# Kernel optimization log

Hardware: AMD Instinct MI355X
Metric: run time of the kernel (lower is better)

The kernel has to match this reference:

```python
import jax, jax.numpy as jnp
import numpy as np

N_HEAD = 16
ROPE_BASE = 10000.0


def rope_cos_sin(T, head_dim, dtype):
    inv_freq = 1.0 / (ROPE_BASE ** (jnp.arange(0, head_dim, 2, dtype=jnp.float32) / head_dim))
    t = jnp.arange(T, dtype=jnp.float32)
    freqs = jnp.einsum('i,j->ij', t, inv_freq)          # [T, head_dim/2]
    emb = jnp.concatenate([freqs, freqs], axis=-1)       # [T, head_dim]
    return jnp.cos(emb).astype(dtype), jnp.sin(emb).astype(dtype)


def rotate_half(x):
    h = x.shape[-1] // 2
    return jnp.concatenate([-x[..., h:], x[..., :h]], axis=-1)


def setup_inputs() -> dict:
    key = jax.random.key(0)
    ks = jax.random.split(key, 5)
    B, T, C = 2, 1024, 2048
    s = 0.02
    return {
        'x': jax.random.normal(ks[0], (B, T, C), dtype=jnp.float32),
        'Wq': jax.random.normal(ks[1], (C, C), dtype=jnp.float32) * s,
        'Wk': jax.random.normal(ks[2], (C, C), dtype=jnp.float32) * s,
        'Wv': jax.random.normal(ks[3], (C, C), dtype=jnp.float32) * s,
        'Wo': jax.random.normal(ks[4], (C, C), dtype=jnp.float32) * s,
    }


def reference(x, Wq, Wk, Wv, Wo):
    B, T, C = x.shape
    H = N_HEAD
    D = C // H
    # torch Linear: y = x @ W.T  (W is [out, in])
    q = jnp.einsum('btc,oc->bto', x, Wq).reshape(B, T, H, D).transpose(0, 2, 1, 3)
    k = jnp.einsum('btc,oc->bto', x, Wk).reshape(B, T, H, D).transpose(0, 2, 1, 3)
    v = jnp.einsum('btc,oc->bto', x, Wv).reshape(B, T, H, D).transpose(0, 2, 1, 3)
    cos, sin = rope_cos_sin(T, D, x.dtype)               # [T, D]
    cos = cos[None, None]                                 # [1,1,T,D]
    sin = sin[None, None]
    q = q * cos + rotate_half(q) * sin
    k = k * cos + rotate_half(k) * sin
    scale = 1.0 / jnp.sqrt(jnp.asarray(D, dtype=x.dtype))
    att = jnp.einsum('bhqd,bhkd->bhqk', q, k) * scale    # [B,H,T,T]
    causal = jnp.tril(jnp.ones((T, T), dtype=bool))
    att = jnp.where(causal[None, None], att, jnp.finfo(x.dtype).min)
    att = jax.nn.softmax(att, axis=-1)
    y = jnp.einsum('bhqk,bhkd->bhqd', att, v)            # [B,H,T,D]
    y = y.transpose(0, 2, 1, 3).reshape(B, T, C)
    return jnp.einsum('btc,oc->bto', y, Wo)
```

## Files before the change

### kernel.cpp

```cpp
#include <hip/hip_runtime.h>
#include <stdint.h>

typedef unsigned short u16;
typedef __bf16 bf16x8 __attribute__((ext_vector_type(8)));
typedef float  f32x4  __attribute__((ext_vector_type(4)));

#define B_  2
#define T_  1024
#define C_  2048
#define H_  16
#define D_  128
#define NTENS 4194304

__device__ __forceinline__ u16 f2bf(float f) {
    union { float f; uint32_t u; } v; v.f = f;
    uint32_t r = (v.u + 0x7FFFu + ((v.u >> 16) & 1u)) >> 16;
    return (u16)r;
}
__device__ __forceinline__ float bf2f(u16 h) {
    union { uint32_t u; float f; } v; v.u = ((uint32_t)h) << 16;
    return v.f;
}

__global__ __launch_bounds__(256) void k_convert(
    const float* __restrict__ x, const float* __restrict__ wq,
    const float* __restrict__ wk, const float* __restrict__ wv,
    const float* __restrict__ wo, u16* __restrict__ dst,
    float* __restrict__ ct, float* __restrict__ st)
{
    int z = blockIdx.z;
    if (z == 5) {
        int idx = blockIdx.x * 256 + threadIdx.x;
        if (idx < 65536) {
            int t = idx >> 6, d = idx & 63;
            float inv = expf(-(float)d * (9.210340371976184f / 64.0f));
            float th = (float)t * inv;
            float s, c;
            sincosf(th, &s, &c);
            ct[idx] = c;
            st[idx] = s;
        }
        return;
    }
    const float* src = (z == 0) ? x : (z == 1) ? wq : (z == 2) ? wk : (z == 3) ? wv : wo;
    u16* d = dst + (size_t)z * NTENS;
    size_t i = ((size_t)blockIdx.x * 256 + threadIdx.x) * 4;
    float4 v = *(const float4*)(src + i);
    ushort4 o;
    o.x = f2bf(v.x); o.y = f2bf(v.y); o.z = f2bf(v.z); o.w = f2bf(v.w);
    *(ushort4*)(d + i) = o;
}

__global__ __launch_bounds__(256) void k_transpose_v(
    const u16* __restrict__ vb, u16* __restrict__ vt)
{
    __shared__ u16 L[64 * 136];
    int t0 = blockIdx.x << 6;
    int bh = blockIdx.y, b = bh >> 4, h = bh & 15;
    const u16* src = vb + (size_t)b * (T_ * C_) + h * D_;
    u16* dst = vt + (size_t)bh * (D_ * T_);
    int tid = threadIdx.x;
#pragma unroll
    for (int i = 0; i < 4; ++i) {
        int idx = (i << 8) + tid;
        int r = idx >> 4, s = idx & 15;
        *(uint4*)&L[r * 136 + (s << 3)] =
            *(const uint4*)&src[(size_t)(t0 + r) * C_ + (s << 3)];
    }
    __syncthreads();
#pragma unroll
    for (int i = 0; i < 8; ++i) {
        int idx = (i << 8) + tid;
        int d = idx >> 4, s = idx & 15;
        int t = s << 2;
        ushort4 o;
        o.x = L[(t    ) * 136 + d];
        o.y = L[(t + 1) * 136 + d];
        o.z = L[(t + 2) * 136 + d];
        o.w = L[(t + 3) * 136 + d];
        *(ushort4*)&dst[(size_t)d * T_ + t0 + t] = o;
    }
}

template<int MTILE, int EPI>
__device__ __forceinline__ void gemm_tile_nt(
    const u16* __restrict__ A, int lda,
    const u16* __restrict__ Bp, int ldb,
    void* __restrict__ Cp, int ldc,
    int m0, int n0, int K,
    u16* SMEM, const float* __restrict__ ct, const float* __restrict__ st, int z)
{
    constexpr int MF  = MTILE / 16;
    constexpr int ACH = MTILE / 32;
    u16* As = SMEM;
    u16* Bs = SMEM + MTILE * 64;

    const int tid  = threadIdx.x;
    const int wave = tid >> 6;
    const int lane = tid & 63;
    const int frow = lane & 15;
    const int quad = lane >> 4;

    const int lrow8  = lane >> 3;
    const int slot   = lane & 7;
    const int gchunk = slot ^ lrow8;

    f32x4 acc[MF][2] = {};

    size_t aoff[ACH], boff[4];
#pragma unroll
    for (int i = 0; i < ACH; ++i) {
        int c = (i << 2) + wave;
        int r = (c << 3) + lrow8;
        aoff[i] = (size_t)(m0 + r) * lda + (gchunk << 3);
    }
#pragma unroll
    for (int i = 0; i < 4; ++i) {
        int r = (i << 5) + (wave << 3) + lrow8;
        boff[i] = (size_t)(n0 + r) * ldb + (gchunk << 3);
    }

    for (int kt = 0; kt < K; kt += 64) {
#pragma unroll
        for (int i = 0; i < ACH; ++i) {
            int c = (i << 2) + wave;
            __builtin_amdgcn_global_load_lds(
                (const __attribute__((address_space(1))) void*)(A + aoff[i] + kt),
                (__attribute__((address_space(3))) void*)(As + (c << 9)), 16, 0, 0);
        }
#pragma unroll
        for (int i = 0; i < 4; ++i) {
            int c = (i << 2) + wave;
            __builtin_amdgcn_global_load_lds(
                (const __attribute__((address_space(1))) void*)(Bp + boff[i] + kt),
                (__attribute__((address_space(3))) void*)(Bs + (c << 9)), 16, 0, 0);
        }
        __syncthreads();

#pragma unroll
        for (int ks = 0; ks < 2; ++ks) {
            int lk = (ks << 2) + quad;
            bf16x8 af[MF], bfv[2];
#pragma unroll
            for (int i = 0; i < MF; ++i) {
                int ar = (i << 4) + frow;
                af[i] = *(const bf16x8*)&As[ar * 64 + ((lk ^ (frow & 7)) << 3)];
            }
#pragma unroll
            for (int j = 0; j < 2; ++j) {
                int br = (wave << 4) + (j << 6) + frow;
                bfv[j] = *(const bf16x8*)&Bs[br * 64 + ((lk ^ (frow & 7)) << 3)];
            }
#pragma unroll
            for (int i = 0; i < MF; ++i)
#pragma unroll
                for (int j = 0; j < 2; ++j)
                    acc[i][j] = __builtin_amdgcn_mfma_f32_16x16x32_bf16(
                        af[i], bfv[j], acc[i][j], 0, 0, 0);
        }
        __syncthreads();
    }

    if constexpr (EPI == 2) {
        if (z < 2) {
            const int d = (wave << 4) + frow;
            const float sc = (z == 0) ? 0.08838834764831845f : 1.0f;
            u16* Op = (u16*)Cp;
#pragma unroll
            for (int i = 0; i < MF; ++i)
#pragma unroll
                for (int r = 0; r < 4; ++r) {
                    int m = m0 + (i << 4) + (quad << 2) + r;
                    int t = m & 1023;
                    float c = ct[t * 64 + d], s = st[t * 64 + d];
                    float a = acc[i][0][r], bb = acc[i][1][r];
                    Op[(size_t)m * ldc + n0 + d]      = f2bf((a * c - bb * s) * sc);
                    Op[(size_t)m * ldc + n0 + d + 64] = f2bf((bb * c + a * s) * sc);
                }
            return;
        }
    }

#pragma unroll
    for (int i = 0; i < MF; ++i)
#pragma unroll
        for (int j = 0; j < 2; ++j)
#pragma unroll
            for (int r = 0; r < 4; ++r) {
                int m = m0 + (i << 4) + (quad << 2) + r;
                int n = n0 + (wave << 4) + (j << 6) + frow;
                if constexpr (EPI == 0)
                    ((float*)Cp)[(size_t)m * ldc + n] = acc[i][j][r];
                else
                    ((u16*)Cp)[(size_t)m * ldc + n] = f2bf(acc[i][j][r]);
            }
}

__global__ __launch_bounds__(256) void k_gemm_qkv(
    const u16* __restrict__ xb, const u16* __restrict__ wq,
    const u16* __restrict__ wk, const u16* __restrict__ wv,
    u16* __restrict__ q, u16* __restrict__ k, u16* __restrict__ v,
    const float* __restrict__ ct, const float* __restrict__ st)
{
    __shared__ u16 SMEM[64 * 64 + 128 * 64];
    int z = blockIdx.z;
    const u16* Bp = (z == 0) ? wq : (z == 1) ? wk : wv;
    u16* Op       = (z == 0) ? q  : (z == 1) ? k  : v;
    gemm_tile_nt<64, 2>(xb, C_, Bp, C_, Op, C_,
                        blockIdx.y * 64, blockIdx.x * 128, C_, SMEM, ct, st, z);
}

__global__ __launch_bounds__(256) void k_flash(
    const u16* __restrict__ qb, const u16* __restrict__ kb,
    const u16* __restrict__ vt, u16* __restrict__ yb)
{
    __shared__ u16 Ks[128 * 128];
    __shared__ u16 Vs[128 * 128];

    const int bx  = blockIdx.x;
    const int bh  = bx & 31, b = bh >> 4, h = bh & 15;
    const int qt  = (bx < 256) ? (15 - (bx >> 5)) : ((bx >> 5) - 8);
    const int KT  = (qt >> 1) + 1;
    const int tid = threadIdx.x, wave = tid >> 6, lane = tid & 63;
    const int frow = lane & 15, quad = lane >> 4;

    const u16* qbase = qb + (size_t)b * (T_ * C_) + h * D_;
    const u16* kbase = kb + (size_t)b * (T_ * C_) + h * D_;
    const u16* vbase = vt + (size_t)bh * (D_ * T_);
    const int q0 = qt << 6;

    bf16x8 qf[4];
#pragma unroll
    for (int ks = 0; ks < 4; ++ks)
        qf[ks] = *(const bf16x8*)&qbase[(size_t)(q0 + (wave << 4) + frow) * C_
                                        + (ks << 5) + (quad << 3)];

    f32x4 Y[8] = {};
    float mrow[4], lrow[4];
#pragma unroll
    for (int r = 0; r < 4; ++r) { mrow[r] = -3e38f; lrow[r] = 0.f; }

    const int tok = q0 + (wave << 4) + (quad << 2);

    for (int kt = 0; kt < KT; ++kt) {
        const int k0 = kt << 7;
        {
            const int r4 = lane >> 4, s16 = lane & 15;
#pragma unroll
            for (int i = 0; i < 8; ++i) {
                int c = (i << 2) + wave;
                int row = (c << 2) + r4;
                int g = (s16 & 8) | ((s16 & 7) ^ (row & 7));
                __builtin_amdgcn_global_load_lds(
                    (const __attribute__((address_space(1))) void*)(kbase + (size_t)(k0 + row) * C_ + (g << 3)),
                    (__attribute__((address_space(3))) void*)(Ks + (c << 9)), 16, 0, 0);
                __builtin_amdgcn_global_load_lds(
                    (const __attribute__((address_space(1))) void*)(vbase + (size_t)row * T_ + k0 + (g << 3)),
                    (__attribute__((address_space(3))) void*)(Vs + (c << 9)), 16, 0, 0);
            }
        }
        __syncthreads();

        f32x4 S[8] = {};
#pragma unroll
        for (int ks = 0; ks < 4; ++ks) {
            int lk = (ks << 2) + quad;
            int sw = ((lk & 8) | ((lk & 7) ^ (frow & 7))) << 3;
#pragma unroll
            for (int jj = 0; jj < 8; ++jj) {
                bf16x8 bb = *(const bf16x8*)&Ks[((jj << 4) + frow) * 128 + sw];
                S[jj] = __builtin_amdgcn_mfma_f32_16x16x32_bf16(qf[ks], bb, S[jj], 0, 0, 0);
            }
        }

        if (kt == KT - 1) {
#pragma unroll
            for (int jj = 0; jj < 8; ++jj) {
                int colg = k0 + (jj << 4) + frow;
#pragma unroll
                for (int r = 0; r < 4; ++r)
                    if (colg > tok + r) S[jj][r] = -1e30f;
            }
        }

        float al[4];
#pragma unroll
        for (int r = 0; r < 4; ++r) {
            float tm = -3e38f;
#pragma unroll
            for (int jj = 0; jj < 8; ++jj) tm = fmaxf(tm, S[jj][r]);
#pragma unroll
            for (int off = 8; off > 0; off >>= 1) tm = fmaxf(tm, __shfl_xor(tm, off));
            float mn = fmaxf(mrow[r], tm);
            al[r] = __expf(mrow[r] - mn);
            mrow[r] = mn;
            float rs = 0.f;
#pragma unroll
            for (int jj = 0; jj < 8; ++jj) {
                float e = __expf(S[jj][r] - mn);
                S[jj][r] = e;
                rs += e;
            }
#pragma unroll
            for (int off = 8; off > 0; off >>= 1) rs += __shfl_xor(rs, off);
            lrow[r] = lrow[r] * al[r] + rs;
        }
#pragma unroll
        for (int dj = 0; dj < 8; ++dj)
#pragma unroll
            for (int r = 0; r < 4; ++r) Y[dj][r] *= al[r];

        __syncthreads();

        u16* Ps = Ks;
#pragma unroll
        for (int jj = 0; jj < 8; ++jj)
#pragma unroll
            for (int r = 0; r < 4; ++r)
                Ps[((wave << 4) + (quad << 2) + r) * 136 + (jj << 4) + frow] = f2bf(S[jj][r]);

#pragma unroll
        for (int ks = 0; ks < 4; ++ks) {
            bf16x8 pa = *(const bf16x8*)&Ps[((wave << 4) + frow) * 136 + (ks << 5) + (quad << 3)];
            int lk = (ks << 2) + quad;
            int sw = ((lk & 8) | ((lk & 7) ^ (frow & 7))) << 3;
#pragma unroll
            for (int dj = 0; dj < 8; ++dj) {
                bf16x8 vv = *(const bf16x8*)&Vs[((dj << 4) + frow) * 128 + sw];
                Y[dj] = __builtin_amdgcn_mfma_f32_16x16x32_bf16(pa, vv, Y[dj], 0, 0, 0);
            }
        }
        __syncthreads();
    }

    u16* ybase = yb + (size_t)b * (T_ * C_) + h * D_;
#pragma unroll
    for (int r = 0; r < 4; ++r) {
        float inv = 1.0f / lrow[r];
#pragma unroll
        for (int dj = 0; dj < 8; ++dj)
            ybase[(size_t)(tok + r) * C_ + (dj << 4) + frow] = f2bf(Y[dj][r] * inv);
    }
}

__global__ __launch_bounds__(256) void k_gemm_out(
    const u16* __restrict__ yb, const u16* __restrict__ wo, float* __restrict__ out)
{
    __shared__ u16 SMEM[64 * 64 + 128 * 64];
    gemm_tile_nt<64, 0>(yb, C_, wo, C_, out, C_,
                        blockIdx.y * 64, blockIdx.x * 128, C_, SMEM, nullptr, nullptr, 0);
}

extern "C" void kernel_launch(void* const* d_in, const int* in_sizes, int n_in,
                              void* d_out, int out_size, void* d_ws, size_t ws_size,
                              hipStream_t stream)
{
    (void)in_sizes; (void)n_in; (void)out_size; (void)ws_size;
    const float* x  = (const float*)d_in[0];
    const float* Wq = (const float*)d_in[1];
    const float* Wk = (const float*)d_in[2];
    const float* Wv = (const float*)d_in[3];
    const float* Wo = (const float*)d_in[4];

    u16* ws  = (u16*)d_ws;
    u16* xb  = ws;
    u16* wqb = ws + (size_t)1 * NTENS;
    u16* wkb = ws + (size_t)2 * NTENS;
    u16* wvb = ws + (size_t)3 * NTENS;
    u16* wob = ws + (size_t)4 * NTENS;
    u16* qb  = ws + (size_t)5 * NTENS;
    u16* kb  = ws + (size_t)6 * NTENS;
    u16* vb  = ws + (size_t)7 * NTENS;
    u16* yb  = ws + (size_t)8 * NTENS;
    u16* vt  = ws + (size_t)9 * NTENS;
    float* ct = (float*)(ws + (size_t)10 * NTENS);
    float* st = ct + 65536;

    k_convert    <<<dim3(4096, 1, 6), 256, 0, stream>>>(x, Wq, Wk, Wv, Wo, ws, ct, st);
    k_gemm_qkv   <<<dim3(16, 32, 3), 256, 0, stream>>>(xb, wqb, wkb, wvb, qb, kb, vb, ct, st);
    k_transpose_v<<<dim3(16, 32), 256, 0, stream>>>(vb, vt);
    k_flash      <<<dim3(512), 256, 0, stream>>>(qb, kb, vt, yb);
    k_gemm_out   <<<dim3(16, 32, 1), 256, 0, stream>>>(yb, wob, (float*)d_out);
}
```

Baseline: 252.6 us.

## Fuse V transpose into QKV GEMM epilogue and enlarge M tile to 128

The V projection epilogue now writes its output directly in transposed per-head [D,T] layout, so the separate transpose kernel and the extra V buffer round trip are gone. The QKV GEMM also moves from 64-row to 128-row tiles, which halves the grid in M and gives more reuse of each weight tile per block. The transposed stores are 4-element vectors strided by T, which may coalesce less well. The larger tile raises register and LDS use per block and leaves fewer blocks to fill the GPU.

Result: slower. 277.6 us (+9.9%).

```diff
diff --git a/kernel.cpp b/kernel.cpp
--- a/kernel.cpp
+++ b/kernel.cpp
@@ -51,37 +51,6 @@
     *(ushort4*)(d + i) = o;
 }
 
-__global__ __launch_bounds__(256) void k_transpose_v(
-    const u16* __restrict__ vb, u16* __restrict__ vt)
-{
-    __shared__ u16 L[64 * 136];
-    int t0 = blockIdx.x << 6;
-    int bh = blockIdx.y, b = bh >> 4, h = bh & 15;
-    const u16* src = vb + (size_t)b * (T_ * C_) + h * D_;
-    u16* dst = vt + (size_t)bh * (D_ * T_);
-    int tid = threadIdx.x;
-#pragma unroll
-    for (int i = 0; i < 4; ++i) {
-        int idx = (i << 8) + tid;
-        int r = idx >> 4, s = idx & 15;
-        *(uint4*)&L[r * 136 + (s << 3)] =
-            *(const uint4*)&src[(size_t)(t0 + r) * C_ + (s << 3)];
-    }
-    __syncthreads();
-#pragma unroll
-    for (int i = 0; i < 8; ++i) {
-        int idx = (i << 8) + tid;
-        int d = idx >> 4, s = idx & 15;
-        int t = s << 2;
-        ushort4 o;
-        o.x = L[(t    ) * 136 + d];
-        o.y = L[(t + 1) * 136 + d];
-        o.z = L[(t + 2) * 136 + d];
-        o.w = L[(t + 3) * 136 + d];
-        *(ushort4*)&dst[(size_t)d * T_ + t0 + t] = o;
-    }
-}
-
 template<int MTILE, int EPI>
 __device__ __forceinline__ void gemm_tile_nt(
     const u16* __restrict__ A, int lda,
@@ -179,6 +148,22 @@
                 }
             return;
         }
+        const int hh = n0 >> 7;
+        const int bI = m0 >> 10;
+        const int t0 = m0 & 1023;
+        u16* Vp = (u16*)Cp + ((size_t)((bI << 4) + hh)) * (D_ * T_);
+#pragma unroll
+        for (int i = 0; i < MF; ++i)
+#pragma unroll
+            for (int j = 0; j < 2; ++j) {
+                int d = (wave << 4) + (j << 6) + frow;
+                int t = t0 + (i << 4) + (quad << 2);
+                ushort4 o;
+                o.x = f2bf(acc[i][j][0]); o.y = f2bf(acc[i][j][1]);
+                o.z = f2bf(acc[i][j][2]); o.w = f2bf(acc[i][j][3]);
+                *(ushort4*)&Vp[(size_t)d * T_ + t] = o;
+            }
+        return;
     }
 
 #pragma unroll
@@ -199,15 +184,15 @@
 __global__ __launch_bounds__(256) void k_gemm_qkv(
     const u16* __restrict__ xb, const u16* __restrict__ wq,
     const u16* __restrict__ wk, const u16* __restrict__ wv,
-    u16* __restrict__ q, u16* __restrict__ k, u16* __restrict__ v,
+    u16* __restrict__ q, u16* __restrict__ k, u16* __restrict__ vt,
     const float* __restrict__ ct, const float* __restrict__ st)
 {
-    __shared__ u16 SMEM[64 * 64 + 128 * 64];
+    __shared__ u16 SMEM[128 * 64 + 128 * 64];
     int z = blockIdx.z;
     const u16* Bp = (z == 0) ? wq : (z == 1) ? wk : wv;
-    u16* Op       = (z == 0) ? q  : (z == 1) ? k  : v;
-    gemm_tile_nt<64, 2>(xb, C_, Bp, C_, Op, C_,
-                        blockIdx.y * 64, blockIdx.x * 128, C_, SMEM, ct, st, z);
+    u16* Op       = (z == 0) ? q  : (z == 1) ? k  : vt;
+    gemm_tile_nt<128, 2>(xb, C_, Bp, C_, Op, C_,
+                         blockIdx.y * 128, blockIdx.x * 128, C_, SMEM, ct, st, z);
 }
 
 __global__ __launch_bounds__(256) void k_flash(
@@ -370,15 +355,13 @@
     u16* wob = ws + (size_t)4 * NTENS;
     u16* qb  = ws + (size_t)5 * NTENS;
     u16* kb  = ws + (size_t)6 * NTENS;
-    u16* vb  = ws + (size_t)7 * NTENS;
     u16* yb  = ws + (size_t)8 * NTENS;
     u16* vt  = ws + (size_t)9 * NTENS;
     float* ct = (float*)(ws + (size_t)10 * NTENS);
     float* st = ct + 65536;
 
-    k_convert    <<<dim3(4096, 1, 6), 256, 0, stream>>>(x, Wq, Wk, Wv, Wo, ws, ct, st);
-    k_gemm_qkv   <<<dim3(16, 32, 3), 256, 0, stream>>>(xb, wqb, wkb, wvb, qb, kb, vb, ct, st);
-    k_transpose_v<<<dim3(16, 32), 256, 0, stream>>>(vb, vt);
-    k_flash      <<<dim3(512), 256, 0, stream>>>(qb, kb, vt, yb);
-    k_gemm_out   <<<dim3(16, 32, 1), 256, 0, stream>>>(yb, wob, (float*)d_out);
-}
+    k_convert <<<dim3(4096, 1, 6), 256, 0, stream>>>(x, Wq, Wk, Wv, Wo, ws, ct, st);
+    k_gemm_qkv<<<dim3(16, 16, 3), 256, 0, stream>>>(xb, wqb, wkb, wvb, qb, kb, vt, ct, st);
+    k_flash   <<<dim3(512), 256, 0, stream>>>(qb, kb, vt, yb);
+    k_gemm_out<<<dim3(16, 32, 1), 256, 0, stream>>>(yb, wob, (float*)d_out);
+}
```
